# Kernel optimization log

Hardware: AMD Instinct MI355X
Metric: run time of the kernel (lower is better)

## Reference

```python
import jax, jax.numpy as jnp
import numpy as np
from jax import lax

M1 = M2 = M3 = 8  # Fourier modes per axis


def _corners(x):
    # gather the 4 low-frequency corner blocks -> [B, C, 2*M1, 2*M2, M3]
    top = jnp.concatenate([x[:, :, :M1, :M2, :M3], x[:, :, -M1:, :M2, :M3]], axis=2)
    bot = jnp.concatenate([x[:, :, :M1, -M2:, :M3], x[:, :, -M1:, -M2:, :M3]], axis=2)
    return jnp.concatenate([top, bot], axis=3)


def _scatter(template, xm):
    # place the mixed corner blocks back into a zero spectrum shaped like template
    xp = jnp.zeros_like(template)
    xp = xp.at[:, :, :M1, :M2, :M3].set(xm[:, :, :M1, :M2, :M3])
    xp = xp.at[:, :, -M1:, :M2, :M3].set(xm[:, :, -M1:, :M2, :M3])
    xp = xp.at[:, :, :M1, -M2:, :M3].set(xm[:, :, :M1, -M2:, :M3])
    xp = xp.at[:, :, -M1:, -M2:, :M3].set(xm[:, :, -M1:, -M2:, :M3])
    return xp


def _spectral_conv(x, w):
    # x: complex [B,C,X,Y,Zr]; w: real [Ci,Co,16,16,14]
    xm = _corners(x)                                    # [B,C,16,16,8] complex
    xr = jnp.fft.irfftn(xm, axes=(-3, -2, -1))          # [B,C,16,16,14] real
    y = jnp.einsum('bixyz,ioxyz->boxyz', xr, w)         # per-point channel mix
    ym = jnp.fft.rfftn(y, axes=(-3, -2, -1))            # [B,C,16,16,8] complex
    return _scatter(x, ym.astype(x.dtype))


def _cgelu(z):
    # torch: complex(gelu(real), gelu(imag)); F.gelu default is exact erf
    return lax.complex(jax.nn.gelu(z.real, approximate=False),
                       jax.nn.gelu(z.imag, approximate=False))


def _cmix(x, wr, wi):
    # einsum 'bi...,io...->bo...' with [Ci,Co,1,1,1] complex pointwise weight
    return jnp.einsum('bixyz,io->boxyz', x, lax.complex(wr, wi))


def setup_inputs() -> dict:
    key = jax.random.key(0)
    ks = jax.random.split(key, 12)
    B, X, Y, Zr = 4, 64, 64, 33
    W = 20
    inp = {
        'x_r': jax.random.normal(ks[0], (B, 3, X, Y, Zr), jnp.float32),
        'x_i': jax.random.normal(ks[1], (B, 3, X, Y, Zr), jnp.float32),
        'smooth': jax.random.uniform(ks[2], (1, 1, X, Y, Zr), jnp.float32),
        'wconv': 0.001 * jax.random.uniform(ks[3], (4, W, W, 2 * M1, 2 * M2, 2 * M3 - 2), jnp.float32),
        'wpt_r': 0.1 * jax.random.uniform(ks[4], (4, W, W), jnp.float32),
        'wpt_i': 0.1 * jax.random.uniform(ks[5], (4, W, W), jnp.float32),
        'fc0_r': 0.1 * jax.random.uniform(ks[6], (3, W), jnp.float32),
        'fc0_i': 0.1 * jax.random.uniform(ks[7], (3, W), jnp.float32),
        'fc1_r': 0.1 * jax.random.uniform(ks[8], (W, 128), jnp.float32),
        'fc1_i': 0.1 * jax.random.uniform(ks[9], (W, 128), jnp.float32),
        'fc2_r': 0.1 * jax.random.uniform(ks[10], (128, 3), jnp.float32),
        'fc2_i': 0.1 * jax.random.uniform(ks[11], (128, 3), jnp.float32),
    }
    return inp


def reference(x_r, x_i, smooth, wconv, wpt_r, wpt_i, fc0_r, fc0_i,
              fc1_r, fc1_i, fc2_r, fc2_i):
    x = lax.complex(x_r, x_i)                     # [B,3,64,64,33] complex64
    x = _cmix(x, fc0_r, fc0_i)                    # lift to width=20
    for l in range(4):
        x1 = _spectral_conv(x, wconv[l])
        x2 = _cmix(x, wpt_r[l], wpt_i[l])
        x = (x1 + x2) * smooth                    # real smoother broadcast
        if l < 3:
            x = _cgelu(x)
    x = _cmix(x, fc1_r, fc1_i)                    # 20 -> 128
    x = _cgelu(x)
    x = _cmix(x, fc2_r, fc2_i)                    # 128 -> 3
    return x
```

## Files before the change

kernel.cpp:

```cpp
#include <hip/hip_runtime.h>
#include <hip/hip_bf16.h>
#include <math.h>

#define XYZ 135168
#define W 20
#define NMODE 2048
#define NREAL 3584

__device__ __forceinline__ float k20_erf(float x) {
    float s = (x < 0.f) ? -1.f : 1.f;
    float a = fabsf(x);
    float t = 1.f / fmaf(0.3275911f, a, 1.f);
    float poly = t * fmaf(t, fmaf(t, fmaf(t, fmaf(t, 1.061405429f, -1.453152027f),
                                           1.421413741f), -0.284496736f), 0.254829592f);
    float e = __expf(-a * a);
    return s * (1.f - poly * e);
}
__device__ __forceinline__ float k20_gelu(float v) {
    return 0.5f * v * (1.0f + k20_erf(v * 0.7071067811865476f));
}

__global__ __launch_bounds__(256, 2)
void k20_fc0(const float* __restrict__ xr_in, const float* __restrict__ xi_in,
             const float* __restrict__ fr, const float* __restrict__ fi,
             float* __restrict__ xre, float* __restrict__ xim) {
    int idx = blockIdx.x * blockDim.x + threadIdx.x;
    if (idx >= 4 * XYZ) return;
    int b = idx / XYZ, p = idx % XYZ;
    float ar[3], ai[3];
#pragma unroll
    for (int i = 0; i < 3; i++) {
        ar[i] = xr_in[(size_t)(b * 3 + i) * XYZ + p];
        ai[i] = xi_in[(size_t)(b * 3 + i) * XYZ + p];
    }
#pragma unroll
    for (int o = 0; o < W; o++) {
        float rr = 0.f, ii = 0.f;
#pragma unroll
        for (int i = 0; i < 3; i++) {
            float wr = fr[i * W + o], wi = fi[i * W + o];
            rr += ar[i] * wr - ai[i] * wi;
            ii += ar[i] * wi + ai[i] * wr;
        }
        xre[(size_t)(b * W + o) * XYZ + p] = rr;
        xim[(size_t)(b * W + o) * XYZ + p] = ii;
    }
}

__global__ __launch_bounds__(256, 2)
void k20_gifftx(const float* __restrict__ xre, const float* __restrict__ xim,
                float* __restrict__ are, float* __restrict__ aim) {
    int t = blockIdx.x * blockDim.x + threadIdx.x;
    if (t >= 80 * NMODE) return;
    int kz = t & 7, ky = (t >> 3) & 15, nx = (t >> 7) & 15, bc = t >> 11;
    int col = (ky < 8) ? ky : ky + 48;
    const float* pr = xre + (size_t)bc * XYZ;
    const float* pi = xim + (size_t)bc * XYZ;
    float accr = 0.f, acci = 0.f;
    for (int kx = 0; kx < 16; kx++) {
        int row = (kx < 8) ? kx : kx + 48;
        int off = (row * 64 + col) * 33 + kz;
        float vr = pr[off], vi = pi[off];
        int m = (kx * nx) & 15;
        float s, c;
        sincosf((float)m * 0.39269908169872414f, &s, &c);
        accr += vr * c - vi * s;
        acci += vr * s + vi * c;
    }
    are[t] = accr * 0.0625f;
    aim[t] = acci * 0.0625f;
}

__global__ __launch_bounds__(256, 2)
void k20_iffty(const float* __restrict__ are, const float* __restrict__ aim,
               float* __restrict__ bre, float* __restrict__ bim) {
    int t = blockIdx.x * blockDim.x + threadIdx.x;
    if (t >= 80 * NMODE) return;
    int kz = t & 7, ny = (t >> 3) & 15, nx = (t >> 7) & 15, bc = t >> 11;
    int base = ((bc * 16 + nx) * 16) * 8 + kz;
    float accr = 0.f, acci = 0.f;
    for (int ky = 0; ky < 16; ky++) {
        float vr = are[base + ky * 8], vi = aim[base + ky * 8];
        int m = (ky * ny) & 15;
        float s, c;
        sincosf((float)m * 0.39269908169872414f, &s, &c);
        accr += vr * c - vi * s;
        acci += vr * s + vi * c;
    }
    bre[t] = accr * 0.0625f;
    bim[t] = acci * 0.0625f;
}

__global__ __launch_bounds__(256, 2)
void k20_irfftz(const float* __restrict__ bre, const float* __restrict__ bim,
                float* __restrict__ r1) {
    int t = blockIdx.x * blockDim.x + threadIdx.x;
    if (t >= 80 * NREAL) return;
    int nz = t % 14;
    int q = t / 14;
    int base = q * 8;
    float acc = bre[base];
    float re7 = bre[base + 7];
    acc += (nz & 1) ? -re7 : re7;
    for (int k = 1; k < 7; k++) {
        int m = (k * nz) % 14;
        float s, c;
        sincosf((float)m * 0.4487989505128276f, &s, &c);
        acc += 2.f * (bre[base + k] * c - bim[base + k] * s);
    }
    r1[t] = acc * (1.0f / 14.0f);
}

__global__ __launch_bounds__(256, 2)
void k20_mix(const float* __restrict__ r1, const float* __restrict__ wconv,
             int l, float* __restrict__ r2) {
    int t = blockIdx.x * blockDim.x + threadIdx.x;
    if (t >= 80 * NREAL) return;
    int p = t % NREAL;
    int o = (t / NREAL) % W;
    int b = t / (NREAL * W);
    const float* wl = wconv + (size_t)l * W * W * NREAL;
    float acc = 0.f;
#pragma unroll
    for (int i = 0; i < W; i++)
        acc += r1[(size_t)(b * W + i) * NREAL + p] * wl[(size_t)(i * W + o) * NREAL + p];
    r2[t] = acc;
}

__global__ __launch_bounds__(256, 2)
void k20_rfftz(const float* __restrict__ r2,
               float* __restrict__ are, float* __restrict__ aim) {
    int t = blockIdx.x * blockDim.x + threadIdx.x;
    if (t >= 80 * NMODE) return;
    int k = t & 7;
    int q = t >> 3;
    int base = q * 14;
    float accr = 0.f, acci = 0.f;
    for (int n = 0; n < 14; n++) {
        float v = r2[base + n];
        int m = (k * n) % 14;
        float s, c;
        sincosf((float)m * 0.4487989505128276f, &s, &c);
        accr += v * c;
        acci -= v * s;
    }
    are[t] = accr;
    aim[t] = acci;
}

__global__ __launch_bounds__(256, 2)
void k20_fftx(const float* __restrict__ are, const float* __restrict__ aim,
              float* __restrict__ bre, float* __restrict__ bim) {
    int t = blockIdx.x * blockDim.x + threadIdx.x;
    if (t >= 80 * NMODE) return;
    int kz = t & 7, ny = (t >> 3) & 15, kx = (t >> 7) & 15, bc = t >> 11;
    int base = bc * 2048 + ny * 8 + kz;
    float accr = 0.f, acci = 0.f;
    for (int nx = 0; nx < 16; nx++) {
        float vr = are[base + nx * 128], vi = aim[base + nx * 128];
        int m = (kx * nx) & 15;
        float s, c;
        sincosf((float)m * 0.39269908169872414f, &s, &c);
        accr += vr * c + vi * s;
        acci += vi * c - vr * s;
    }
    bre[t] = accr;
    bim[t] = acci;
}

__global__ __launch_bounds__(256, 2)
void k20_ffty(const float* __restrict__ bre, const float* __restrict__ bim,
              float* __restrict__ are, float* __restrict__ aim) {
    int t = blockIdx.x * blockDim.x + threadIdx.x;
    if (t >= 80 * NMODE) return;
    int kz = t & 7, ky = (t >> 3) & 15, kx = (t >> 7) & 15, bc = t >> 11;
    int base = bc * 2048 + kx * 128 + kz;
    float accr = 0.f, acci = 0.f;
    for (int ny = 0; ny < 16; ny++) {
        float vr = bre[base + ny * 8], vi = bim[base + ny * 8];
        int m = (ky * ny) & 15;
        float s, c;
        sincosf((float)m * 0.39269908169872414f, &s, &c);
        accr += vr * c + vi * s;
        acci += vi * c - vr * s;
    }
    are[t] = accr;
    aim[t] = acci;
}

__global__ __launch_bounds__(256, 2)
void k20_combine(float* __restrict__ xre, float* __restrict__ xim,
                 const float* __restrict__ ere, const float* __restrict__ eim,
                 const float* __restrict__ wpt_r, const float* __restrict__ wpt_i,
                 int l, const float* __restrict__ smooth, int apply_gelu) {
    __shared__ float wr[W * W], wi[W * W];
    for (int i = threadIdx.x; i < W * W; i += blockDim.x) {
        wr[i] = wpt_r[l * W * W + i];
        wi[i] = wpt_i[l * W * W + i];
    }
    __syncthreads();
    int idx = blockIdx.x * blockDim.x + threadIdx.x;
    if (idx >= 4 * XYZ) return;
    int b = idx / XYZ, p = idx % XYZ;
    int gz = p % 33;
    int gxy = p / 33;
    int gy = gxy & 63;
    int gx = gxy >> 6;
    int kx = (gx < 8) ? gx : ((gx >= 56) ? gx - 48 : -1);
    int ky = (gy < 8) ? gy : ((gy >= 56) ? gy - 48 : -1);
    bool corner = (kx >= 0) && (ky >= 0) && (gz < 8);
    float sm = smooth[p];
    float ar[W], ai[W];
#pragma unroll
    for (int i = 0; i < W; i++) {
        ar[i] = xre[(size_t)(b * W + i) * XYZ + p];
        ai[i] = xim[(size_t)(b * W + i) * XYZ + p];
    }
    int ebase = corner ? (b * W * NMODE + (kx * 16 + ky) * 8 + gz) : 0;
    for (int o = 0; o < W; o++) {
        float rr = 0.f, ii = 0.f;
#pragma unroll
        for (int i = 0; i < W; i++) {
            float wwr = wr[i * W + o], wwi = wi[i * W + o];
            rr += ar[i] * wwr - ai[i] * wwi;
            ii += ar[i] * wwi + ai[i] * wwr;
        }
        if (corner) {
            rr += ere[ebase + o * NMODE];
            ii += eim[ebase + o * NMODE];
        }
        rr *= sm;
        ii *= sm;
        if (apply_gelu) {
            rr = k20_gelu(rr);
            ii = k20_gelu(ii);
        }
        xre[(size_t)(b * W + o) * XYZ + p] = rr;
        xim[(size_t)(b * W + o) * XYZ + p] = ii;
    }
}

__global__ __launch_bounds__(256, 2)
void k20_tail(const float* __restrict__ xre, const float* __restrict__ xim,
              const float* __restrict__ f1r, const float* __restrict__ f1i,
              const float* __restrict__ f2r, const float* __restrict__ f2i,
              float* __restrict__ outf) {
    __shared__ __align__(16) float w1r[W * 128], w1i[W * 128];
    __shared__ __align__(16) float w2r[3 * 128], w2i[3 * 128];
    for (int i = threadIdx.x; i < W * 128; i += blockDim.x) {
        w1r[i] = f1r[i];
        w1i[i] = f1i[i];
    }
    for (int i = threadIdx.x; i < 3 * 128; i += blockDim.x) {
        int j = i & 127, o = i >> 7;
        w2r[o * 128 + j] = f2r[j * 3 + o];
        w2i[o * 128 + j] = f2i[j * 3 + o];
    }
    __syncthreads();
    int idx = blockIdx.x * blockDim.x + threadIdx.x;
    if (idx >= 4 * XYZ) return;
    int b = idx / XYZ, p = idx % XYZ;
    float ar[W], ai[W];
#pragma unroll
    for (int i = 0; i < W; i++) {
        ar[i] = xre[(size_t)(b * W + i) * XYZ + p];
        ai[i] = xim[(size_t)(b * W + i) * XYZ + p];
    }
    float accr[3] = {0.f, 0.f, 0.f};
    for (int jc = 0; jc < 16; jc++) {
        int jb = jc * 8;
        float tr[8], ti[8];
#pragma unroll
        for (int jj = 0; jj < 8; jj++) { tr[jj] = 0.f; ti[jj] = 0.f; }
#pragma unroll 1
        for (int i = 0; i < W; i++) {
            float4 wrA = *(const float4*)&w1r[i * 128 + jb];
            float4 wrB = *(const float4*)&w1r[i * 128 + jb + 4];
            float4 wiA = *(const float4*)&w1i[i * 128 + jb];
            float4 wiB = *(const float4*)&w1i[i * 128 + jb + 4];
            float xr_ = ar[i], xi_ = ai[i];
            tr[0] += xr_ * wrA.x - xi_ * wiA.x;  ti[0] += xr_ * wiA.x + xi_ * wrA.x;
            tr[1] += xr_ * wrA.y - xi_ * wiA.y;  ti[1] += xr_ * wiA.y + xi_ * wrA.y;
            tr[2] += xr_ * wrA.z - xi_ * wiA.z;  ti[2] += xr_ * wiA.z + xi_ * wrA.z;
            tr[3] += xr_ * wrA.w - xi_ * wiA.w;  ti[3] += xr_ * wiA.w + xi_ * wrA.w;
            tr[4] += xr_ * wrB.x - xi_ * wiB.x;  ti[4] += xr_ * wiB.x + xi_ * wrB.x;
            tr[5] += xr_ * wrB.y - xi_ * wiB.y;  ti[5] += xr_ * wiB.y + xi_ * wrB.y;
            tr[6] += xr_ * wrB.z - xi_ * wiB.z;  ti[6] += xr_ * wiB.z + xi_ * wrB.z;
            tr[7] += xr_ * wrB.w - xi_ * wiB.w;  ti[7] += xr_ * wiB.w + xi_ * wrB.w;
        }
#pragma unroll
        for (int jj = 0; jj < 8; jj++) {
            tr[jj] = k20_gelu(tr[jj]);
            ti[jj] = k20_gelu(ti[jj]);
        }
#pragma unroll
        for (int o = 0; o < 3; o++) {
            float4 crA = *(const float4*)&w2r[o * 128 + jb];
            float4 crB = *(const float4*)&w2r[o * 128 + jb + 4];
            float4 ciA = *(const float4*)&w2i[o * 128 + jb];
            float4 ciB = *(const float4*)&w2i[o * 128 + jb + 4];
            accr[o] += tr[0] * crA.x - ti[0] * ciA.x;
            accr[o] += tr[1] * crA.y - ti[1] * ciA.y;
            accr[o] += tr[2] * crA.z - ti[2] * ciA.z;
            accr[o] += tr[3] * crA.w - ti[3] * ciA.w;
            accr[o] += tr[4] * crB.x - ti[4] * ciB.x;
            accr[o] += tr[5] * crB.y - ti[5] * ciB.y;
            accr[o] += tr[6] * crB.z - ti[6] * ciB.z;
            accr[o] += tr[7] * crB.w - ti[7] * ciB.w;
        }
    }
#pragma unroll
    for (int o = 0; o < 3; o++) {
        size_t k = (size_t)(b * 3 + o) * XYZ + p;
        outf[k] = __bfloat162float(__float2bfloat16(accr[o]));
    }
}

extern "C" void kernel_launch(void* const* d_in, const int* in_sizes, int n_in,
                              void* d_out, int out_size, void* d_ws, size_t ws_size,
                              hipStream_t stream) {
    const float* x_r    = (const float*)d_in[0];
    const float* x_i    = (const float*)d_in[1];
    const float* smooth = (const float*)d_in[2];
    const float* wconv  = (const float*)d_in[3];
    const float* wpt_r  = (const float*)d_in[4];
    const float* wpt_i  = (const float*)d_in[5];
    const float* fc0_r  = (const float*)d_in[6];
    const float* fc0_i  = (const float*)d_in[7];
    const float* fc1_r  = (const float*)d_in[8];
    const float* fc1_i  = (const float*)d_in[9];
    const float* fc2_r  = (const float*)d_in[10];
    const float* fc2_i  = (const float*)d_in[11];
    float* outf = (float*)d_out;

    const size_t NBW = (size_t)4 * W * XYZ;
    const size_t NM  = (size_t)80 * NMODE;
    const size_t NR  = (size_t)80 * NREAL;
    const size_t modeFloats = 4 * NM + 2 * NR;

    float* modebuf = (float*)d_ws;
    float* are = modebuf;
    float* aim = are + NM;
    float* bre = aim + NM;
    float* bim = bre + NM;
    float* r1  = bim + NM;
    float* r2  = r1 + NR;
    float* xre = modebuf + modeFloats;
    float* xim = xre + NBW;

    dim3 blk(256);
    const int gP = (4 * XYZ) / 256;
    const int gM = (80 * NMODE) / 256;
    const int gR = (80 * NREAL) / 256;

    k20_fc0<<<gP, blk, 0, stream>>>(x_r, x_i, fc0_r, fc0_i, xre, xim);
    for (int l = 0; l < 4; l++) {
        k20_gifftx<<<gM, blk, 0, stream>>>(xre, xim, are, aim);
        k20_iffty<<<gM, blk, 0, stream>>>(are, aim, bre, bim);
        k20_irfftz<<<gR, blk, 0, stream>>>(bre, bim, r1);
        k20_mix<<<gR, blk, 0, stream>>>(r1, wconv, l, r2);
        k20_rfftz<<<gM, blk, 0, stream>>>(r2, are, aim);
        k20_fftx<<<gM, blk, 0, stream>>>(are, aim, bre, bim);
        k20_ffty<<<gM, blk, 0, stream>>>(bre, bim, are, aim);
        k20_combine<<<gP, blk, 0, stream>>>(xre, xim, are, aim, wpt_r, wpt_i, l,
                                            smooth, (l < 3) ? 1 : 0);
    }
    k20_tail<<<gP, blk, 0, stream>>>(xre, xim, fc1_r, fc1_i, fc2_r, fc2_i, outf);
}
```

Before: 749.4 us.

## Fuse per-channel spectral transform stages into shared-memory kernels

```diff
diff --git a/kernel.cpp b/kernel.cpp
--- a/kernel.cpp
+++ b/kernel.cpp
@@ -7,7 +7,7 @@
 #define NMODE 2048
 #define NREAL 3584
 
-__device__ __forceinline__ float k20_erf(float x) {
+__device__ __forceinline__ float m21_erf(float x) {
     float s = (x < 0.f) ? -1.f : 1.f;
     float a = fabsf(x);
     float t = 1.f / fmaf(0.3275911f, a, 1.f);
@@ -16,12 +16,12 @@
     float e = __expf(-a * a);
     return s * (1.f - poly * e);
 }
-__device__ __forceinline__ float k20_gelu(float v) {
-    return 0.5f * v * (1.0f + k20_erf(v * 0.7071067811865476f));
-}
-
-__global__ __launch_bounds__(256, 2)
-void k20_fc0(const float* __restrict__ xr_in, const float* __restrict__ xi_in,
+__device__ __forceinline__ float m21_gelu(float v) {
+    return 0.5f * v * (1.0f + m21_erf(v * 0.7071067811865476f));
+}
+
+__global__ __launch_bounds__(256, 4)
+void m21_fc0(const float* __restrict__ xr_in, const float* __restrict__ xi_in,
              const float* __restrict__ fr, const float* __restrict__ fi,
              float* __restrict__ xre, float* __restrict__ xim) {
     int idx = blockIdx.x * blockDim.x + threadIdx.x;
@@ -48,71 +48,73 @@
 }
 
 __global__ __launch_bounds__(256, 2)
-void k20_gifftx(const float* __restrict__ xre, const float* __restrict__ xim,
-                float* __restrict__ are, float* __restrict__ aim) {
-    int t = blockIdx.x * blockDim.x + threadIdx.x;
-    if (t >= 80 * NMODE) return;
-    int kz = t & 7, ky = (t >> 3) & 15, nx = (t >> 7) & 15, bc = t >> 11;
-    int col = (ky < 8) ? ky : ky + 48;
+void m21_spec_inv(const float* __restrict__ xre, const float* __restrict__ xim,
+                  float* __restrict__ r1) {
+    __shared__ float s0r[2048], s0i[2048], s1r[2048], s1i[2048];
+    int bc = blockIdx.x;
+    int tid = threadIdx.x;
     const float* pr = xre + (size_t)bc * XYZ;
     const float* pi = xim + (size_t)bc * XYZ;
-    float accr = 0.f, acci = 0.f;
-    for (int kx = 0; kx < 16; kx++) {
+    for (int t = tid; t < 2048; t += 256) {
+        int kz = t & 7, ky = (t >> 3) & 15, kx = t >> 7;
         int row = (kx < 8) ? kx : kx + 48;
+        int col = (ky < 8) ? ky : ky + 48;
         int off = (row * 64 + col) * 33 + kz;
-        float vr = pr[off], vi = pi[off];
-        int m = (kx * nx) & 15;
-        float s, c;
-        sincosf((float)m * 0.39269908169872414f, &s, &c);
-        accr += vr * c - vi * s;
-        acci += vr * s + vi * c;
-    }
-    are[t] = accr * 0.0625f;
-    aim[t] = acci * 0.0625f;
-}
-
-__global__ __launch_bounds__(256, 2)
-void k20_iffty(const float* __restrict__ are, const float* __restrict__ aim,
-               float* __restrict__ bre, float* __restrict__ bim) {
-    int t = blockIdx.x * blockDim.x + threadIdx.x;
-    if (t >= 80 * NMODE) return;
-    int kz = t & 7, ny = (t >> 3) & 15, nx = (t >> 7) & 15, bc = t >> 11;
-    int base = ((bc * 16 + nx) * 16) * 8 + kz;
-    float accr = 0.f, acci = 0.f;
-    for (int ky = 0; ky < 16; ky++) {
-        float vr = are[base + ky * 8], vi = aim[base + ky * 8];
-        int m = (ky * ny) & 15;
-        float s, c;
-        sincosf((float)m * 0.39269908169872414f, &s, &c);
-        accr += vr * c - vi * s;
-        acci += vr * s + vi * c;
-    }
-    bre[t] = accr * 0.0625f;
-    bim[t] = acci * 0.0625f;
-}
-
-__global__ __launch_bounds__(256, 2)
-void k20_irfftz(const float* __restrict__ bre, const float* __restrict__ bim,
-                float* __restrict__ r1) {
-    int t = blockIdx.x * blockDim.x + threadIdx.x;
-    if (t >= 80 * NREAL) return;
-    int nz = t % 14;
-    int q = t / 14;
-    int base = q * 8;
-    float acc = bre[base];
-    float re7 = bre[base + 7];
-    acc += (nz & 1) ? -re7 : re7;
-    for (int k = 1; k < 7; k++) {
-        int m = (k * nz) % 14;
-        float s, c;
-        sincosf((float)m * 0.4487989505128276f, &s, &c);
-        acc += 2.f * (bre[base + k] * c - bim[base + k] * s);
-    }
-    r1[t] = acc * (1.0f / 14.0f);
-}
-
-__global__ __launch_bounds__(256, 2)
-void k20_mix(const float* __restrict__ r1, const float* __restrict__ wconv,
+        s0r[t] = pr[off];
+        s0i[t] = pi[off];
+    }
+    __syncthreads();
+    for (int t = tid; t < 2048; t += 256) {
+        int kz = t & 7, ky = (t >> 3) & 15, nx = t >> 7;
+        int base = ky * 8 + kz;
+        float accr = 0.f, acci = 0.f;
+        for (int kx = 0; kx < 16; kx++) {
+            float vr = s0r[base + kx * 128], vi = s0i[base + kx * 128];
+            int m = (kx * nx) & 15;
+            float s, c;
+            sincosf((float)m * 0.39269908169872414f, &s, &c);
+            accr += vr * c - vi * s;
+            acci += vr * s + vi * c;
+        }
+        s1r[t] = accr * 0.0625f;
+        s1i[t] = acci * 0.0625f;
+    }
+    __syncthreads();
+    for (int t = tid; t < 2048; t += 256) {
+        int kz = t & 7, ny = (t >> 3) & 15, nx = t >> 7;
+        int base = nx * 128 + kz;
+        float accr = 0.f, acci = 0.f;
+        for (int ky = 0; ky < 16; ky++) {
+            float vr = s1r[base + ky * 8], vi = s1i[base + ky * 8];
+            int m = (ky * ny) & 15;
+            float s, c;
+            sincosf((float)m * 0.39269908169872414f, &s, &c);
+            accr += vr * c - vi * s;
+            acci += vr * s + vi * c;
+        }
+        s0r[t] = accr * 0.0625f;
+        s0i[t] = acci * 0.0625f;
+    }
+    __syncthreads();
+    for (int t = tid; t < 3584; t += 256) {
+        int nz = t % 14;
+        int q = t / 14;
+        int base = q * 8;
+        float acc = s0r[base];
+        float re7 = s0r[base + 7];
+        acc += (nz & 1) ? -re7 : re7;
+        for (int k = 1; k < 7; k++) {
+            int m = (k * nz) % 14;
+            float s, c;
+            sincosf((float)m * 0.4487989505128276f, &s, &c);
+            acc += 2.f * (s0r[base + k] * c - s0i[base + k] * s);
+        }
+        r1[(size_t)bc * 3584 + t] = acc * (1.0f / 14.0f);
+    }
+}
+
+__global__ __launch_bounds__(256, 4)
+void m21_mix(const float* __restrict__ r1, const float* __restrict__ wconv,
              int l, float* __restrict__ r2) {
     int t = blockIdx.x * blockDim.x + threadIdx.x;
     if (t >= 80 * NREAL) return;
@@ -128,68 +130,66 @@
 }
 
 __global__ __launch_bounds__(256, 2)
-void k20_rfftz(const float* __restrict__ r2,
-               float* __restrict__ are, float* __restrict__ aim) {
-    int t = blockIdx.x * blockDim.x + threadIdx.x;
-    if (t >= 80 * NMODE) return;
-    int k = t & 7;
-    int q = t >> 3;
-    int base = q * 14;
-    float accr = 0.f, acci = 0.f;
-    for (int n = 0; n < 14; n++) {
-        float v = r2[base + n];
-        int m = (k * n) % 14;
-        float s, c;
-        sincosf((float)m * 0.4487989505128276f, &s, &c);
-        accr += v * c;
-        acci -= v * s;
-    }
-    are[t] = accr;
-    aim[t] = acci;
-}
-
-__global__ __launch_bounds__(256, 2)
-void k20_fftx(const float* __restrict__ are, const float* __restrict__ aim,
-              float* __restrict__ bre, float* __restrict__ bim) {
-    int t = blockIdx.x * blockDim.x + threadIdx.x;
-    if (t >= 80 * NMODE) return;
-    int kz = t & 7, ny = (t >> 3) & 15, kx = (t >> 7) & 15, bc = t >> 11;
-    int base = bc * 2048 + ny * 8 + kz;
-    float accr = 0.f, acci = 0.f;
-    for (int nx = 0; nx < 16; nx++) {
-        float vr = are[base + nx * 128], vi = aim[base + nx * 128];
-        int m = (kx * nx) & 15;
-        float s, c;
-        sincosf((float)m * 0.39269908169872414f, &s, &c);
-        accr += vr * c + vi * s;
-        acci += vi * c - vr * s;
-    }
-    bre[t] = accr;
-    bim[t] = acci;
-}
-
-__global__ __launch_bounds__(256, 2)
-void k20_ffty(const float* __restrict__ bre, const float* __restrict__ bim,
-              float* __restrict__ are, float* __restrict__ aim) {
-    int t = blockIdx.x * blockDim.x + threadIdx.x;
-    if (t >= 80 * NMODE) return;
-    int kz = t & 7, ky = (t >> 3) & 15, kx = (t >> 7) & 15, bc = t >> 11;
-    int base = bc * 2048 + kx * 128 + kz;
-    float accr = 0.f, acci = 0.f;
-    for (int ny = 0; ny < 16; ny++) {
-        float vr = bre[base + ny * 8], vi = bim[base + ny * 8];
-        int m = (ky * ny) & 15;
-        float s, c;
-        sincosf((float)m * 0.39269908169872414f, &s, &c);
-        accr += vr * c + vi * s;
-        acci += vi * c - vr * s;
-    }
-    are[t] = accr;
-    aim[t] = acci;
-}
-
-__global__ __launch_bounds__(256, 2)
-void k20_combine(float* __restrict__ xre, float* __restrict__ xim,
+void m21_spec_fwd(const float* __restrict__ r2,
+                  float* __restrict__ are, float* __restrict__ aim) {
+    __shared__ float sr[3584];
+    __shared__ float c1r[2048], c1i[2048], c2r[2048], c2i[2048];
+    int bc = blockIdx.x;
+    int tid = threadIdx.x;
+    for (int t = tid; t < 3584; t += 256) sr[t] = r2[(size_t)bc * 3584 + t];
+    __syncthreads();
+    for (int t = tid; t < 2048; t += 256) {
+        int k = t & 7;
+        int q = t >> 3;
+        int base = q * 14;
+        float accr = 0.f, acci = 0.f;
+        for (int n = 0; n < 14; n++) {
+            float v = sr[base + n];
+            int m = (k * n) % 14;
+            float s, c;
+            sincosf((float)m * 0.4487989505128276f, &s, &c);
+            accr += v * c;
+            acci -= v * s;
+        }
+        c1r[t] = accr;
+        c1i[t] = acci;
+    }
+    __syncthreads();
+    for (int t = tid; t < 2048; t += 256) {
+        int kz = t & 7, ny = (t >> 3) & 15, kx = t >> 7;
+        int base = ny * 8 + kz;
+        float accr = 0.f, acci = 0.f;
+        for (int nx = 0; nx < 16; nx++) {
+            float vr = c1r[base + nx * 128], vi = c1i[base + nx * 128];
+            int m = (kx * nx) & 15;
+            float s, c;
+            sincosf((float)m * 0.39269908169872414f, &s, &c);
+            accr += vr * c + vi * s;
+            acci += vi * c - vr * s;
+        }
+        c2r[t] = accr;
+        c2i[t] = acci;
+    }
+    __syncthreads();
+    for (int t = tid; t < 2048; t += 256) {
+        int kz = t & 7, ky = (t >> 3) & 15, kx = t >> 7;
+        int base = kx * 128 + kz;
+        float accr = 0.f, acci = 0.f;
+        for (int ny = 0; ny < 16; ny++) {
+            float vr = c2r[base + ny * 8], vi = c2i[base + ny * 8];
+            int m = (ky * ny) & 15;
+            float s, c;
+            sincosf((float)m * 0.39269908169872414f, &s, &c);
+            accr += vr * c + vi * s;
+            acci += vi * c - vr * s;
+        }
+        are[(size_t)bc * 2048 + t] = accr;
+        aim[(size_t)bc * 2048 + t] = acci;
+    }
+}
+
+__global__ __launch_bounds__(256, 4)
+void m21_combine(float* __restrict__ xre, float* __restrict__ xim,
                  const float* __restrict__ ere, const float* __restrict__ eim,
                  const float* __restrict__ wpt_r, const float* __restrict__ wpt_i,
                  int l, const float* __restrict__ smooth, int apply_gelu) {
@@ -232,16 +232,16 @@
         rr *= sm;
         ii *= sm;
         if (apply_gelu) {
-            rr = k20_gelu(rr);
-            ii = k20_gelu(ii);
+            rr = m21_gelu(rr);
+            ii = m21_gelu(ii);
         }
         xre[(size_t)(b * W + o) * XYZ + p] = rr;
         xim[(size_t)(b * W + o) * XYZ + p] = ii;
     }
 }
 
-__global__ __launch_bounds__(256, 2)
-void k20_tail(const float* __restrict__ xre, const float* __restrict__ xim,
+__global__ __launch_bounds__(256, 4)
+void m21_tail(const float* __restrict__ xre, const float* __restrict__ xim,
               const float* __restrict__ f1r, const float* __restrict__ f1i,
               const float* __restrict__ f2r, const float* __restrict__ f2i,
               float* __restrict__ outf) {
@@ -290,8 +290,8 @@
         }
 #pragma unroll
         for (int jj = 0; jj < 8; jj++) {
-            tr[jj] = k20_gelu(tr[jj]);
-            ti[jj] = k20_gelu(ti[jj]);
+            tr[jj] = m21_gelu(tr[jj]);
+            ti[jj] = m21_gelu(ti[jj]);
         }
 #pragma unroll
         for (int o = 0; o < 3; o++) {
@@ -336,34 +336,26 @@
     const size_t NBW = (size_t)4 * W * XYZ;
     const size_t NM  = (size_t)80 * NMODE;
     const size_t NR  = (size_t)80 * NREAL;
-    const size_t modeFloats = 4 * NM + 2 * NR;
 
     float* modebuf = (float*)d_ws;
     float* are = modebuf;
     float* aim = are + NM;
-    float* bre = aim + NM;
-    float* bim = bre + NM;
-    float* r1  = bim + NM;
+    float* r1  = aim + NM;
     float* r2  = r1 + NR;
-    float* xre = modebuf + modeFloats;
+    float* xre = r2 + NR;
     float* xim = xre + NBW;
 
     dim3 blk(256);
     const int gP = (4 * XYZ) / 256;
-    const int gM = (80 * NMODE) / 256;
     const int gR = (80 * NREAL) / 256;
 
-    k20_fc0<<<gP, blk, 0, stream>>>(x_r, x_i, fc0_r, fc0_i, xre, xim);
+    m21_fc0<<<gP, blk, 0, stream>>>(x_r, x_i, fc0_r, fc0_i, xre, xim);
     for (int l = 0; l < 4; l++) {
-        k20_gifftx<<<gM, blk, 0, stream>>>(xre, xim, are, aim);
-        k20_iffty<<<gM, blk, 0, stream>>>(are, aim, bre, bim);
-        k20_irfftz<<<gR, blk, 0, stream>>>(bre, bim, r1);
-        k20_mix<<<gR, blk, 0, stream>>>(r1, wconv, l, r2);
-        k20_rfftz<<<gM, blk, 0, stream>>>(r2, are, aim);
-        k20_fftx<<<gM, blk, 0, stream>>>(are, aim, bre, bim);
-        k20_ffty<<<gM, blk, 0, stream>>>(bre, bim, are, aim);
-        k20_combine<<<gP, blk, 0, stream>>>(xre, xim, are, aim, wpt_r, wpt_i, l,
+        m21_spec_inv<<<80, blk, 0, stream>>>(xre, xim, r1);
+        m21_mix<<<gR, blk, 0, stream>>>(r1, wconv, l, r2);
+        m21_spec_fwd<<<80, blk, 0, stream>>>(r2, are, aim);
+        m21_combine<<<gP, blk, 0, stream>>>(xre, xim, are, aim, wpt_r, wpt_i, l,
                                             smooth, (l < 3) ? 1 : 0);
     }
-    k20_tail<<<gP, blk, 0, stream>>>(xre, xim, fc1_r, fc1_i, fc2_r, fc2_i, outf);
-}
+    m21_tail<<<gP, blk, 0, stream>>>(xre, xim, fc1_r, fc1_i, fc2_r, fc2_i, outf);
+}
```

Result: slower. 1.050 ms (+40.1%).
